# Kernel tuning notes

Measured on AMD Instinct MI355X. Metric: run time of the kernel, lower is better.

The kernel has to match this reference:

```python
import jax, jax.numpy as jnp
import numpy as np
from jax import lax

V, E, H = 32000, 256, 512
B, S, T = 32, 128, 64


def setup_inputs() -> dict:
    key = jax.random.key(0)
    ks = iter(jax.random.split(key, 32))
    p = lambda shape: jax.random.normal(next(ks), shape, jnp.float32) * 0.05
    inp = {
        "src": jax.random.randint(next(ks), (B, S), 0, V),
        "target": jax.random.randint(next(ks), (B, T), 0, V),
        "enc_emb": p((V, E)),
        "enc_Wih_f": p((3 * H, E)), "enc_Whh_f": p((3 * H, H)),
        "enc_bih_f": p((3 * H,)), "enc_bhh_f": p((3 * H,)),
        "enc_Wih_b": p((3 * H, E)), "enc_Whh_b": p((3 * H, H)),
        "enc_bih_b": p((3 * H,)), "enc_bhh_b": p((3 * H,)),
        "enc_fc_W": p((H, 2 * H)), "enc_fc_b": p((H,)),
        "dec_emb": p((V, E)),
        "attn_W": p((H, 3 * H)), "attn_b": p((H,)), "attn_v": p((H,)),
        "dec_Wih": p((3 * H, E + 2 * H)), "dec_Whh": p((3 * H, H)),
        "dec_bih": p((3 * H,)), "dec_bhh": p((3 * H,)),
        "fc1_W": p((V, 3 * H + E)), "fc1_b": p((V,)),
    }
    return inp


def gru_cell(h, x, Wih, Whh, bih, bhh):
    # PyTorch GRU cell. h:[B,H], x:[B,I]
    gx = x @ Wih.T + bih
    gh = h @ Whh.T + bhh
    xr, xz, xn = jnp.split(gx, 3, axis=-1)
    hr, hz, hn = jnp.split(gh, 3, axis=-1)
    r = jax.nn.sigmoid(xr + hr)
    z = jax.nn.sigmoid(xz + hz)
    n = jnp.tanh(xn + r * hn)
    return (1.0 - z) * n + z * h


def reference(src, target, enc_emb, enc_Wih_f, enc_Whh_f, enc_bih_f, enc_bhh_f,
              enc_Wih_b, enc_Whh_b, enc_bih_b, enc_bhh_b, enc_fc_W, enc_fc_b,
              dec_emb, attn_W, attn_b, attn_v, dec_Wih, dec_Whh, dec_bih,
              dec_bhh, fc1_W, fc1_b):
    src_t = src.T          # [S, B]
    tgt_t = target.T       # [T, B]
    batch = src.shape[0]
    hdim = enc_fc_b.shape[0]
    vocab = fc1_b.shape[0]
    tlen = target.shape[1]

    # ---- Encoder: bidirectional single-layer GRU ----
    x = enc_emb[src_t]     # [S, B, E]
    h0 = jnp.zeros((batch, hdim), x.dtype)

    def step_f(h, xt):
        h2 = gru_cell(h, xt, enc_Wih_f, enc_Whh_f, enc_bih_f, enc_bhh_f)
        return h2, h2

    def step_b(h, xt):
        h2 = gru_cell(h, xt, enc_Wih_b, enc_Whh_b, enc_bih_b, enc_bhh_b)
        return h2, h2

    hf, out_f = lax.scan(step_f, h0, x)
    hb, out_b_rev = lax.scan(step_b, h0, x[::-1])
    out_b = out_b_rev[::-1]
    enc_out = jnp.concatenate([out_f, out_b], axis=-1)        # [S, B, 2H]
    hidden = jnp.tanh(jnp.concatenate([hf, hb], axis=-1) @ enc_fc_W.T + enc_fc_b)  # [B, H]

    mask = (src != 0)                                          # [B, S]
    enc_bt = enc_out.transpose(1, 0, 2)                        # [B, S, 2H]
    # split additive-attention weight: cat order is (hidden, enc_out)
    W_h, W_e = attn_W[:, :hdim], attn_W[:, hdim:]
    enc_proj = jnp.einsum('bsd,hd->bsh', enc_bt, W_e)          # precompute [B,S,H]

    # ---- Decoder loop (teacher_ratio = 1.0 -> always teacher forcing) ----
    def dec_step(h, inp_tok):
        emb = dec_emb[inp_tok]                                 # [B, E]
        energy = jnp.tanh((h @ W_h.T)[:, None, :] + enc_proj + attn_b)  # [B,S,H]
        scores = energy @ attn_v                               # [B, S]
        scores = jnp.where(mask, scores, jnp.float32(-1e10))
        a = jax.nn.softmax(scores, axis=1)
        weighted = jnp.einsum('bs,bsd->bd', a, enc_bt)         # [B, 2H]
        gin = jnp.concatenate([emb, weighted], axis=-1)        # [B, E+2H]
        h2 = gru_cell(h, gin, dec_Wih, dec_Whh, dec_bih, dec_bhh)
        out = jnp.concatenate([h2, emb, weighted], axis=-1) @ fc1_W.T + fc1_b  # [B,V]
        return h2, (out, jnp.argmax(out, axis=1))

    _, (outs, preds) = lax.scan(dec_step, hidden, tgt_t[:-1])  # outs: [T-1, B, V]

    outputs = jnp.zeros((batch, tlen, vocab), outs.dtype).at[:, :tlen - 1, :].set(
        outs.transpose(1, 0, 2))
    preds_full = jnp.zeros((batch, tlen), jnp.float32).at[:, :tlen - 1].set(
        preds.T.astype(jnp.float32))
    return outputs, preds_full
```

## Files before the change

### kernel.cpp

```cpp
#include <hip/hip_runtime.h>

#define V_ 32000
#define E_ 256
#define H_ 512
#define B_ 32
#define S_ 128
#define T_ 64
#define TD_ 63
#define G3_ 1536
#define CATK_ 1792
#define DIN_ 1280
#define MPAD_ 2048

typedef __attribute__((ext_vector_type(8))) short bf16x8;
typedef __attribute__((ext_vector_type(4))) float f32x4;

__device__ inline unsigned short bf16_rne(float x) {
    unsigned u = __float_as_uint(x);
    unsigned r = u + 0x7FFFu + ((u >> 16) & 1u);
    return (unsigned short)(r >> 16);
}

__device__ __forceinline__ float ato_ldf(const float* p) {
    return __hip_atomic_load((const float*)p, __ATOMIC_RELAXED, __HIP_MEMORY_SCOPE_AGENT);
}
__device__ __forceinline__ void ato_stf(float* p, float v) {
    __hip_atomic_store(p, v, __ATOMIC_RELAXED, __HIP_MEMORY_SCOPE_AGENT);
}

__device__ __forceinline__ void fast_barN(unsigned* base, int idx, unsigned ngroups)
{
    asm volatile("s_waitcnt vmcnt(0)" ::: "memory");
    __syncthreads();
    if (threadIdx.x == 0) {
        unsigned* gcnt = base + (idx >> 4) * 64;
        unsigned* ggen = gcnt + 32;
        unsigned* tcnt = base + ngroups * 64;
        unsigned* tgen = tcnt + 32;
        unsigned g0 = __hip_atomic_load(ggen, __ATOMIC_RELAXED, __HIP_MEMORY_SCOPE_AGENT);
        unsigned a  = __hip_atomic_fetch_add(gcnt, 1u, __ATOMIC_RELAXED, __HIP_MEMORY_SCOPE_AGENT);
        if (a == 15u) {
            unsigned t0 = __hip_atomic_load(tgen, __ATOMIC_RELAXED, __HIP_MEMORY_SCOPE_AGENT);
            unsigned ta = __hip_atomic_fetch_add(tcnt, 1u, __ATOMIC_RELAXED, __HIP_MEMORY_SCOPE_AGENT);
            if (ta == ngroups - 1u) {
                __hip_atomic_store(tcnt, 0u, __ATOMIC_RELAXED, __HIP_MEMORY_SCOPE_AGENT);
                __hip_atomic_store(tgen, t0 + 1u, __ATOMIC_RELAXED, __HIP_MEMORY_SCOPE_AGENT);
            } else {
                while (__hip_atomic_load(tgen, __ATOMIC_RELAXED, __HIP_MEMORY_SCOPE_AGENT) == t0)
                    __builtin_amdgcn_s_sleep(1);
            }
            __hip_atomic_store(gcnt, 0u, __ATOMIC_RELAXED, __HIP_MEMORY_SCOPE_AGENT);
            __hip_atomic_store(ggen, g0 + 1u, __ATOMIC_RELAXED, __HIP_MEMORY_SCOPE_AGENT);
        } else {
            while (__hip_atomic_load(ggen, __ATOMIC_RELAXED, __HIP_MEMORY_SCOPE_AGENT) == g0)
                __builtin_amdgcn_s_sleep(1);
        }
    }
    __syncthreads();
}

__global__ __launch_bounds__(256)
void prep_kernel(const int* __restrict__ src, const int* __restrict__ tgt,
                 int* __restrict__ tokf, int* __restrict__ tokb, int* __restrict__ tokd,
                 float* __restrict__ enc_h0, unsigned* __restrict__ bars)
{
    int tid = blockIdx.x * 256 + threadIdx.x;
    if (tid < S_ * B_) {
        int s = tid >> 5, b = tid & 31;
        tokf[tid] = src[b * S_ + s];
        tokb[tid] = src[b * S_ + (S_ - 1 - s)];
    }
    if (tid < TD_ * B_) {
        int t = tid >> 5, b = tid & 31;
        tokd[tid] = tgt[b * T_ + t];
    }
    if (tid < 2 * B_ * H_) enc_h0[tid] = 0.f;
    if (tid < 4096) bars[tid] = 0u;
}

__global__ __launch_bounds__(256)
void emb_cat_kernel(const int* __restrict__ tokd, const float* __restrict__ dec_emb,
                    float* __restrict__ cat)
{
    int row = blockIdx.x;
    int tid = threadIdx.x;
    cat[(size_t)row * CATK_ + H_ + tid] = dec_emb[(size_t)tokd[row] * E_ + tid];
}

template<int GATHER, int FC1MAP>
__global__ __launch_bounds__(256)
void gemm128_kernel(const float* __restrict__ A, int lda,
                    const int* __restrict__ tokens, const float* __restrict__ emb,
                    const float* __restrict__ W, int ldw,
                    const float* __restrict__ bias,
                    float* __restrict__ C, int ldc,
                    int M, int N, int K)
{
    __shared__ float As[16][132];
    __shared__ float Ws[16][132];
    (void)N;
    int tid = threadIdx.x;
    int m0 = blockIdx.y * 128, n0 = blockIdx.x * 128;
    int tx = tid & 15, ty = tid >> 4;
    float c[8][8];
#pragma unroll
    for (int i = 0; i < 8; i++)
#pragma unroll
        for (int j = 0; j < 8; j++) c[i][j] = 0.f;

    int arow = tid >> 1;
    int kq = (tid & 1) * 8;

    int am = m0 + arow; if (am >= M) am = M - 1;
    const float* arp;
    if (GATHER) arp = emb + (size_t)tokens[am] * (size_t)K;
    else        arp = A + (size_t)am * (size_t)lda;
    const float* wrp = W + (size_t)(n0 + arow) * (size_t)ldw;

    for (int kb = 0; kb < K; kb += 16) {
        __syncthreads();
        float4 a0 = *(const float4*)(arp + kb + kq);
        float4 a1 = *(const float4*)(arp + kb + kq + 4);
        float4 w0 = *(const float4*)(wrp + kb + kq);
        float4 w1 = *(const float4*)(wrp + kb + kq + 4);
        As[kq + 0][arow] = a0.x; As[kq + 1][arow] = a0.y;
        As[kq + 2][arow] = a0.z; As[kq + 3][arow] = a0.w;
        As[kq + 4][arow] = a1.x; As[kq + 5][arow] = a1.y;
        As[kq + 6][arow] = a1.z; As[kq + 7][arow] = a1.w;
        Ws[kq + 0][arow] = w0.x; Ws[kq + 1][arow] = w0.y;
        Ws[kq + 2][arow] = w0.z; Ws[kq + 3][arow] = w0.w;
        Ws[kq + 4][arow] = w1.x; Ws[kq + 5][arow] = w1.y;
        Ws[kq + 6][arow] = w1.z; Ws[kq + 7][arow] = w1.w;
        __syncthreads();
#pragma unroll
        for (int kk = 0; kk < 16; kk++) {
            float a[8], bb[8];
            *(float4*)&a[0]  = *(const float4*)&As[kk][ty * 8];
            *(float4*)&a[4]  = *(const float4*)&As[kk][ty * 8 + 4];
            *(float4*)&bb[0] = *(const float4*)&Ws[kk][tx * 8];
            *(float4*)&bb[4] = *(const float4*)&Ws[kk][tx * 8 + 4];
#pragma unroll
            for (int i = 0; i < 8; i++)
#pragma unroll
                for (int j = 0; j < 8; j++) c[i][j] += a[i] * bb[j];
        }
    }

#pragma unroll
    for (int i = 0; i < 8; i++) {
        int m = m0 + ty * 8 + i;
        if (m < M) {
            size_t rowoff;
            if (FC1MAP) { int tt = m >> 5, bb2 = m & 31; rowoff = ((size_t)bb2 * T_ + tt) * (size_t)ldc; }
            else        rowoff = (size_t)m * (size_t)ldc;
#pragma unroll
            for (int j = 0; j < 8; j += 4) {
                int n = n0 + tx * 8 + j;
                float4 v;
                v.x = c[i][j + 0] + bias[n + 0];
                v.y = c[i][j + 1] + bias[n + 1];
                v.z = c[i][j + 2] + bias[n + 2];
                v.w = c[i][j + 3] + bias[n + 3];
                *(float4*)(C + rowoff + n) = v;
            }
        }
    }
}

__global__ __launch_bounds__(256)
void enc_coop_kernel(const float* __restrict__ gxf, const float* __restrict__ gxb,
                     const float* __restrict__ Whh_f, const float* __restrict__ bhh_f,
                     const float* __restrict__ Whh_b, const float* __restrict__ bhh_b,
                     float* __restrict__ encrot, float* __restrict__ enc_bt,
                     const float* __restrict__ fcW, const float* __restrict__ fcb,
                     float* __restrict__ hT0, unsigned* __restrict__ bars)
{
    const int bid = blockIdx.x;
    const int dir = bid >> 6, bh = (bid >> 5) & 1, kc = bid & 31;
    const int tid = threadIdx.x;
    const int bl = tid & 15, kl = tid >> 4;
    const int b = bh * 16 + bl, k = kc * 16 + kl;
    const float* Whh = dir ? Whh_b : Whh_f;
    const float* bhhp = dir ? bhh_b : bhh_f;
    const float* gx  = dir ? gxb : gxf;
    __shared__ float hL[16 * 516];
    const float* wr = Whh + (size_t)k * H_;
    const float* wz = Whh + (size_t)(H_ + k) * H_;
    const float* wn = Whh + (size_t)(2 * H_ + k) * H_;
    const float b_r = bhhp[k], b_z = bhhp[H_ + k], b_n = bhhp[2 * H_ + k];
    unsigned* dbar = bars + dir * 512;
    const int idx = bid & 63;

    for (int t = 0; t < S_; ++t) {
        const float* hin = encrot + (size_t)t * (2 * B_ * H_) + (size_t)dir * (B_ * H_);
        float* hout = encrot + (size_t)(t + 1) * (2 * B_ * H_) + (size_t)dir * (B_ * H_);
        const float* hsrc = hin + (size_t)bh * 16 * H_;
        for (int i = tid * 4; i < 16 * H_; i += 1024) {
            int r = i >> 9, cix = i & 511;
            *(float4*)&hL[r * 516 + cix] = *(const float4*)(hsrc + i);
        }
        __syncthreads();
        float ar = 0.f, az = 0.f, an = 0.f;
        const float* hv = &hL[bl * 516];
#pragma unroll 4
        for (int j = 0; j < H_; j += 4) {
            float4 h4 = *(const float4*)(hv + j);
            float4 r4 = *(const float4*)(wr + j);
            float4 z4 = *(const float4*)(wz + j);
            float4 n4 = *(const float4*)(wn + j);
            ar += h4.x * r4.x + h4.y * r4.y + h4.z * r4.z + h4.w * r4.w;
            az += h4.x * z4.x + h4.y * z4.y + h4.z * z4.z + h4.w * z4.w;
            an += h4.x * n4.x + h4.y * n4.y + h4.z * n4.z + h4.w * n4.w;
        }
        const float* gxr = gx + ((size_t)t * B_ + b) * G3_;
        float xr = gxr[k], xz = gxr[H_ + k], xn = gxr[2 * H_ + k];
        float rg = 1.f / (1.f + expf(-(xr + ar + b_r)));
        float zg = 1.f / (1.f + expf(-(xz + az + b_z)));
        float ng = tanhf(xn + rg * (an + b_n));
        float hp = hL[bl * 516 + k];
        float h2 = (1.f - zg) * ng + zg * hp;
        ato_stf(hout + (size_t)b * H_ + k, h2);
        int s_out = dir ? (S_ - 1 - t) : t;
        enc_bt[((size_t)b * S_ + s_out) * (2 * H_) + dir * H_ + k] = h2;
        fast_barN(dbar, idx, 4);
    }
    fast_barN(bars + 1024, bid, 8);

    {
        const int b2 = bid & 31, ih = bid >> 5;
        float* hc = hL;
        const float* hfin = encrot + (size_t)S_ * (2 * B_ * H_);
        const float* hf  = hfin + (size_t)b2 * H_;
        const float* hbk = hfin + (size_t)B_ * H_ + (size_t)b2 * H_;
        for (int i = tid; i < H_; i += 256) { hc[i] = hf[i]; hc[H_ + i] = hbk[i]; }
        __syncthreads();
        if (tid < 128) {
            int i = ih * 128 + tid;
            const float* w = fcW + (size_t)i * (2 * H_);
            float acc = 0.f;
            for (int j = 0; j < 2 * H_; j += 4) {
                float4 a4 = *(const float4*)&hc[j];
                float4 w4 = *(const float4*)(w + j);
                acc += a4.x * w4.x + a4.y * w4.y + a4.z * w4.z + a4.w * w4.w;
            }
            ato_stf(hT0 + (size_t)b2 * H_ + i, tanhf(acc + fcb[i]));
        }
    }
}

__global__ __launch_bounds__(256)
void dec_coop_kernel(const float* __restrict__ attn_W, const float* __restrict__ attn_v,
                     const float* __restrict__ enc_projB, const float* __restrict__ enc_bt,
                     const int* __restrict__ src,
                     const float* __restrict__ dWhh, const float* __restrict__ dbhh,
                     const float* __restrict__ dWih, const float* __restrict__ gx_emb,
                     float* __restrict__ cat, float* __restrict__ hT,
                     float* __restrict__ hwhT, float* __restrict__ wT,
                     float* __restrict__ wpart, float* __restrict__ mlq,
                     unsigned* __restrict__ bars)
{
    const int bid = blockIdx.x, tid = threadIdx.x;
    const int bp = bid >> 4, kr = bid & 15;
    const int b0 = bp * 2, b1 = b0 + 1;
    const int k0 = kr * 32;
    __shared__ float hA[512], hB[512];
    __shared__ float ghhA[96], ghhB[96];
    __shared__ float xwA[96], xwB[96];
    __shared__ float wA[1024], wB[1024];
    __shared__ float hwhL[512], vL[512], sL[32], eS[32], cmb[8];

    const int p1act = (kr < 8);
    const int p1q   = kr & 3;
    const int p1b_  = b0 + (kr >> 2);
    const int cact  = (kr == 8 || kr == 9);
    const int cb    = b0 + (kr - 8);
    const int r0 = tid >> 1, b2_0 = tid & 1;

    for (int t = 0; t < TD_; ++t) {
        const int pp = t & 1;
        const float* hin = hT + (size_t)pp * (B_ * H_);
        float* hout = hT + (size_t)(1 - pp) * (B_ * H_);
        float* cat_t = cat + (size_t)t * B_ * CATK_;

        for (int j = tid; j < H_; j += 256) {
            hA[j] = ato_ldf(hin + (size_t)b0 * H_ + j);
            hB[j] = ato_ldf(hin + (size_t)b1 * H_ + j);
        }
        __syncthreads();
        {
            const float* hv = b2_0 ? hB : hA;
            const float* wrow;
            if (r0 < 32) wrow = attn_W + (size_t)(k0 + r0) * G3_;
            else {
                int rr = r0 - 32;
                wrow = dWhh + (size_t)((rr >> 5) * H_ + k0 + (rr & 31)) * H_;
            }
            float a0 = 0.f, a1 = 0.f;
            for (int j = 0; j < H_; j += 8) {
                float4 w0 = *(const float4*)(wrow + j);
                float4 w1 = *(const float4*)(wrow + j + 4);
                float4 h0 = *(const float4*)&hv[j];
                float4 h1 = *(const float4*)&hv[j + 4];
                a0 += w0.x * h0.x + w0.y * h0.y + w0.z * h0.z + w0.w * h0.w;
                a1 += w1.x * h1.x + w1.y * h1.y + w1.z * h1.z + w1.w * h1.w;
            }
            float acc = a0 + a1;
            int b = b2_0 ? b1 : b0;
            if (r0 < 32) ato_stf(hwhT + (size_t)b * H_ + k0 + r0, acc);
            else {
                int rr = r0 - 32;
                float* g = b2_0 ? ghhB : ghhA;
                g[rr] = acc + dbhh[(rr >> 5) * H_ + k0 + (rr & 31)];
            }
        }
        fast_barN(bars, bid, 16);

        if (p1act) {
            const int ab = p1b_;
            const int s0 = p1q * 32;
            for (int i = tid; i < H_; i += 256) {
                hwhL[i] = ato_ldf(hwhT + (size_t)ab * H_ + i);
                vL[i] = attn_v[i];
            }
            __syncthreads();
            {
                int s = tid >> 3, u = tid & 7;
                const float* pr = enc_projB + ((size_t)ab * S_ + s0 + s) * H_ + u * 64;
                const float* hwo = hwhL + u * 64;
                const float* vo = vL + u * 64;
                float a0 = 0.f, a1 = 0.f, a2 = 0.f, a3 = 0.f;
#pragma unroll
                for (int i = 0; i < 64; i += 4) {
                    float x0 = hwo[i + 0] + pr[i + 0];
                    float x1 = hwo[i + 1] + pr[i + 1];
                    float x2 = hwo[i + 2] + pr[i + 2];
                    float x3 = hwo[i + 3] + pr[i + 3];
                    a0 += vo[i + 0] * (1.f - 2.f / (__expf(2.f * x0) + 1.f));
                    a1 += vo[i + 1] * (1.f - 2.f / (__expf(2.f * x1) + 1.f));
                    a2 += vo[i + 2] * (1.f - 2.f / (__expf(2.f * x2) + 1.f));
                    a3 += vo[i + 3] * (1.f - 2.f / (__expf(2.f * x3) + 1.f));
                }
                float acc = (a0 + a1) + (a2 + a3);
                acc += __shfl_xor(acc, 1);
                acc += __shfl_xor(acc, 2);
                acc += __shfl_xor(acc, 4);
                if (u == 0) sL[s] = (src[ab * S_ + s0 + s] != 0) ? acc : -1e10f;
            }
            __syncthreads();
            if (tid < 32) {
                float v = sL[tid];
                float m = v;
#pragma unroll
                for (int off = 1; off < 32; off <<= 1) m = fmaxf(m, __shfl_xor(m, off));
                float e = expf(v - m);
                eS[tid] = e;
                float l = e;
#pragma unroll
                for (int off = 1; off < 32; off <<= 1) l += __shfl_xor(l, off);
                if (tid == 0) {
                    ato_stf(mlq + (size_t)(ab * 4 + p1q) * 2 + 0, m);
                    ato_stf(mlq + (size_t)(ab * 4 + p1q) * 2 + 1, l);
                }
            }
            __syncthreads();
            {
                int c4 = tid * 4;
                const float* eb = enc_bt + ((size_t)ab * S_ + s0) * (2 * H_) + c4;
                float4 ac0 = {0, 0, 0, 0}, ac1 = {0, 0, 0, 0};
                float4 ac2 = {0, 0, 0, 0}, ac3 = {0, 0, 0, 0};
                for (int s = 0; s < 32; s += 4) {
                    float4 v0 = *(const float4*)(eb + (size_t)(s + 0) * (2 * H_));
                    float4 v1 = *(const float4*)(eb + (size_t)(s + 1) * (2 * H_));
                    float4 v2 = *(const float4*)(eb + (size_t)(s + 2) * (2 * H_));
                    float4 v3 = *(const float4*)(eb + (size_t)(s + 3) * (2 * H_));
                    float e0 = eS[s], e1 = eS[s + 1], e2 = eS[s + 2], e3 = eS[s + 3];
                    ac0.x += e0 * v0.x; ac0.y += e0 * v0.y; ac0.z += e0 * v0.z; ac0.w += e0 * v0.w;
                    ac1.x += e1 * v1.x; ac1.y += e1 * v1.y; ac1.z += e1 * v1.z; ac1.w += e1 * v1.w;
                    ac2.x += e2 * v2.x; ac2.y += e2 * v2.y; ac2.z += e2 * v2.z; ac2.w += e2 * v2.w;
                    ac3.x += e3 * v3.x; ac3.y += e3 * v3.y; ac3.z += e3 * v3.z; ac3.w += e3 * v3.w;
                }
                float* dst = wpart + (size_t)(ab * 4 + p1q) * 1024 + c4;
                ato_stf(dst + 0, (ac0.x + ac1.x) + (ac2.x + ac3.x));
                ato_stf(dst + 1, (ac0.y + ac1.y) + (ac2.y + ac3.y));
                ato_stf(dst + 2, (ac0.z + ac1.z) + (ac2.z + ac3.z));
                ato_stf(dst + 3, (ac0.w + ac1.w) + (ac2.w + ac3.w));
            }
        }
        fast_barN(bars, bid, 16);

        if (cact) {
            const int ab = cb;
            if (tid < 4) {
                cmb[tid] = ato_ldf(mlq + (size_t)(ab * 4 + tid) * 2 + 0);
                cmb[4 + tid] = ato_ldf(mlq + (size_t)(ab * 4 + tid) * 2 + 1);
            }
            __syncthreads();
            float m = fmaxf(fmaxf(cmb[0], cmb[1]), fmaxf(cmb[2], cmb[3]));
            float e0 = expf(cmb[0] - m), e1 = expf(cmb[1] - m);
            float e2 = expf(cmb[2] - m), e3 = expf(cmb[3] - m);
            float L = e0 * cmb[4] + e1 * cmb[5] + e2 * cmb[6] + e3 * cmb[7];
            float inv = 1.f / L;
            int c4 = tid * 4;
            const float* p0 = wpart + (size_t)(ab * 4 + 0) * 1024 + c4;
            const float* p1 = wpart + (size_t)(ab * 4 + 1) * 1024 + c4;
            const float* p2 = wpart + (size_t)(ab * 4 + 2) * 1024 + c4;
            const float* p3 = wpart + (size_t)(ab * 4 + 3) * 1024 + c4;
            float4 w4;
            w4.x = (e0 * ato_ldf(p0 + 0) + e1 * ato_ldf(p1 + 0) + e2 * ato_ldf(p2 + 0) + e3 * ato_ldf(p3 + 0)) * inv;
            w4.y = (e0 * ato_ldf(p0 + 1) + e1 * ato_ldf(p1 + 1) + e2 * ato_ldf(p2 + 1) + e3 * ato_ldf(p3 + 1)) * inv;
            w4.z = (e0 * ato_ldf(p0 + 2) + e1 * ato_ldf(p1 + 2) + e2 * ato_ldf(p2 + 2) + e3 * ato_ldf(p3 + 2)) * inv;
            w4.w = (e0 * ato_ldf(p0 + 3) + e1 * ato_ldf(p1 + 3) + e2 * ato_ldf(p2 + 3) + e3 * ato_ldf(p3 + 3)) * inv;
            ato_stf(wT + (size_t)ab * 1024 + c4 + 0, w4.x);
            ato_stf(wT + (size_t)ab * 1024 + c4 + 1, w4.y);
            ato_stf(wT + (size_t)ab * 1024 + c4 + 2, w4.z);
            ato_stf(wT + (size_t)ab * 1024 + c4 + 3, w4.w);
            *(float4*)(cat_t + (size_t)ab * CATK_ + (H_ + E_) + c4) = w4;
        }
        fast_barN(bars, bid, 16);

        for (int c = tid; c < 2 * H_; c += 256) {
            wA[c] = ato_ldf(wT + (size_t)b0 * 1024 + c);
            wB[c] = ato_ldf(wT + (size_t)b1 * 1024 + c);
        }
        __syncthreads();
        if (tid < 192) {
            int rr = tid >> 1, b2 = tid & 1;
            const float* wv = b2 ? wB : wA;
            const float* wrow = dWih + (size_t)((rr >> 5) * H_ + k0 + (rr & 31)) * DIN_ + E_;
            float a0 = 0.f, a1 = 0.f;
            for (int c = 0; c < 2 * H_; c += 8) {
                float4 w0 = *(const float4*)(wrow + c);
                float4 w1 = *(const float4*)(wrow + c + 4);
                float4 x0 = *(const float4*)&wv[c];
                float4 x1 = *(const float4*)&wv[c + 4];
                a0 += w0.x * x0.x + w0.y * x0.y + w0.z * x0.z + w0.w * x0.w;
                a1 += w1.x * x1.x + w1.y * x1.y + w1.z * x1.z + w1.w * x1.w;
            }
            (b2 ? xwB : xwA)[rr] = a0 + a1;
        }
        __syncthreads();
        if (tid < 64) {
            int b2 = tid >> 5, kk = tid & 31;
            int b = b2 ? b1 : b0;
            int k = k0 + kk;
            const float* g = b2 ? ghhB : ghhA;
            const float* x = b2 ? xwB : xwA;
            float hr = g[kk], hz = g[32 + kk], hn = g[64 + kk];
            float xr = x[kk], xz = x[32 + kk], xn = x[64 + kk];
            const float* gxe = gx_emb + ((size_t)t * B_ + b) * G3_;
            float rg = 1.f / (1.f + expf(-(gxe[k] + xr + hr)));
            float zg = 1.f / (1.f + expf(-(gxe[H_ + k] + xz + hz)));
            float ng = tanhf(gxe[2 * H_ + k] + xn + rg * hn);
            float hp = b2 ? hB[k] : hA[k];
            float h2 = (1.f - zg) * ng + zg * hp;
            ato_stf(hout + (size_t)b * H_ + k, h2);
            cat_t[(size_t)b * CATK_ + k] = h2;
        }
        fast_barN(bars, bid, 16);
    }
}

__global__ __launch_bounds__(256)
void splitA_kernel(const float* __restrict__ cat,
                   unsigned short* __restrict__ Ahi, unsigned short* __restrict__ Alo)
{
    size_t i4 = ((size_t)blockIdx.x * 256 + threadIdx.x) * 4;
    if (i4 >= (size_t)MPAD_ * CATK_) return;
    size_t row = i4 / CATK_;
    float4 v;
    if (row < (size_t)TD_ * B_) v = *(const float4*)(cat + i4);
    else { v.x = v.y = v.z = v.w = 0.f; }
    float f[4] = {v.x, v.y, v.z, v.w};
    unsigned short h[4], l[4];
#pragma unroll
    for (int j = 0; j < 4; j++) {
        h[j] = bf16_rne(f[j]);
        float hf = __uint_as_float((unsigned)h[j] << 16);
        l[j] = bf16_rne(f[j] - hf);
    }
    *(ushort4*)(Ahi + i4) = make_ushort4(h[0], h[1], h[2], h[3]);
    *(ushort4*)(Alo + i4) = make_ushort4(l[0], l[1], l[2], l[3]);
}

__global__ __launch_bounds__(256)
void fc1_mfma_kernel(const unsigned short* __restrict__ Ahi,
                     const unsigned short* __restrict__ Alo,
                     const float* __restrict__ W,
                     const float* __restrict__ bias,
                     float* __restrict__ C)
{
    __shared__ unsigned short lA[2][128][40];
    __shared__ unsigned short lW[2][128][40];
    const int tid = threadIdx.x;
    const int m0 = blockIdx.x * 128, n0 = blockIdx.y * 128;
    const int w = tid >> 6, lane = tid & 63;
    const int wm = w >> 1, wn = w & 1;
    const int frow = lane & 15, fk = (lane >> 4) * 8;

    f32x4 acc[4][4];
#pragma unroll
    for (int mi = 0; mi < 4; mi++)
#pragma unroll
        for (int ni = 0; ni < 4; ni++) acc[mi][ni] = (f32x4){0.f, 0.f, 0.f, 0.f};

    const int srow = tid >> 1;
    const int skq = (tid & 1) * 16;

    const unsigned short* gAhi = Ahi + (size_t)(m0 + srow) * CATK_ + skq;
    const unsigned short* gAlo = Alo + (size_t)(m0 + srow) * CATK_ + skq;
    const float*          gW   = W   + (size_t)(n0 + srow) * CATK_ + skq;

    int4 rAh0, rAh1, rAl0, rAl1;
    float4 rW0, rW1, rW2, rW3;

#define FC1_LOAD(kb)                                        \
    do {                                                    \
        rAh0 = *(const int4*)(gAhi + (kb));                 \
        rAh1 = *(const int4*)(gAhi + (kb) + 8);             \
        rAl0 = *(const int4*)(gAlo + (kb));                 \
        rAl1 = *(const int4*)(gAlo + (kb) + 8);             \
        rW0  = *(const float4*)(gW + (kb));                 \
        rW1  = *(const float4*)(gW + (kb) + 4);             \
        rW2  = *(const float4*)(gW + (kb) + 8);             \
        rW3  = *(const float4*)(gW + (kb) + 12);            \
    } while (0)

    FC1_LOAD(0);

    for (int kb = 0; kb < CATK_; kb += 32) {
        __syncthreads();
        *(int4*)&lA[0][srow][skq]     = rAh0;
        *(int4*)&lA[0][srow][skq + 8] = rAh1;
        *(int4*)&lA[1][srow][skq]     = rAl0;
        *(int4*)&lA[1][srow][skq + 8] = rAl1;
        {
            float f[16] = {rW0.x, rW0.y, rW0.z, rW0.w, rW1.x, rW1.y, rW1.z, rW1.w,
                           rW2.x, rW2.y, rW2.z, rW2.w, rW3.x, rW3.y, rW3.z, rW3.w};
            unsigned hp[8], lp[8];
#pragma unroll
            for (int j = 0; j < 8; j++) {
                float x0 = f[2 * j], x1 = f[2 * j + 1];
                unsigned short h0 = bf16_rne(x0), h1 = bf16_rne(x1);
                float r0 = x0 - __uint_as_float((unsigned)h0 << 16);
                float r1 = x1 - __uint_as_float((unsigned)h1 << 16);
                hp[j] = (unsigned)h0 | ((unsigned)h1 << 16);
                lp[j] = (unsigned)bf16_rne(r0) | ((unsigned)bf16_rne(r1) << 16);
            }
            *(int4*)&lW[0][srow][skq]     = make_int4(hp[0], hp[1], hp[2], hp[3]);
            *(int4*)&lW[0][srow][skq + 8] = make_int4(hp[4], hp[5], hp[6], hp[7]);
            *(int4*)&lW[1][srow][skq]     = make_int4(lp[0], lp[1], lp[2], lp[3]);
            *(int4*)&lW[1][srow][skq + 8] = make_int4(lp[4], lp[5], lp[6], lp[7]);
        }
        __syncthreads();
        if (kb + 32 < CATK_) FC1_LOAD(kb + 32);

        bf16x8 a[2][4];
#pragma unroll
        for (int mi = 0; mi < 4; mi++) {
            int r = wm * 64 + mi * 16 + frow;
            a[0][mi] = *(const bf16x8*)&lA[0][r][fk];
            a[1][mi] = *(const bf16x8*)&lA[1][r][fk];
        }
#pragma unroll
        for (int ni = 0; ni < 4; ni++) {
            int r = wn * 64 + ni * 16 + frow;
            bf16x8 bh = *(const bf16x8*)&lW[0][r][fk];
            bf16x8 bl = *(const bf16x8*)&lW[1][r][fk];
#pragma unroll
            for (int mi = 0; mi < 4; mi++) {
                acc[mi][ni] = __builtin_amdgcn_mfma_f32_16x16x32_bf16(a[0][mi], bh, acc[mi][ni], 0, 0, 0);
                acc[mi][ni] = __builtin_amdgcn_mfma_f32_16x16x32_bf16(a[1][mi], bh, acc[mi][ni], 0, 0, 0);
                acc[mi][ni] = __builtin_amdgcn_mfma_f32_16x16x32_bf16(a[0][mi], bl, acc[mi][ni], 0, 0, 0);
            }
        }
    }
#undef FC1_LOAD

#pragma unroll
    for (int ni = 0; ni < 4; ni++) {
        int col = n0 + wn * 64 + ni * 16 + frow;
        float bc = bias[col];
#pragma unroll
        for (int mi = 0; mi < 4; mi++) {
            int mbase = m0 + wm * 64 + mi * 16 + (lane >> 4) * 4;
            f32x4 v = acc[mi][ni];
#pragma unroll
            for (int r = 0; r < 4; r++) {
                int m = mbase + r;
                if (m < TD_ * B_) {
                    int tt = m >> 5, bb2 = m & 31;
                    C[((size_t)bb2 * T_ + tt) * V_ + col] = v[r] + bc;
                }
            }
        }
    }
}

__global__ __launch_bounds__(256)
void argmax_kernel(const float* __restrict__ outp, float* __restrict__ preds)
{
    int row = blockIdx.x;
    int t = row >> 5, b = row & 31;
    const float* p = outp + ((size_t)b * T_ + t) * V_;
    int tid = threadIdx.x;
    float best = -3.4e38f; int bi = V_;
    for (int i = tid; i < V_; i += 256) {
        float v = p[i];
        if (v > best) { best = v; bi = i; }
    }
    __shared__ float bv[256];
    __shared__ int bidx[256];
    bv[tid] = best; bidx[tid] = bi;
    __syncthreads();
    for (int off = 128; off > 0; off >>= 1) {
        if (tid < off) {
            float v2 = bv[tid + off]; int i2 = bidx[tid + off];
            if (v2 > bv[tid] || (v2 == bv[tid] && i2 < bidx[tid])) { bv[tid] = v2; bidx[tid] = i2; }
        }
        __syncthreads();
    }
    if (tid == 0) preds[(size_t)b * T_ + t] = (float)bidx[0];
}

__global__ __launch_bounds__(256)
void zero_tail_kernel(float* __restrict__ outp, float* __restrict__ preds)
{
    int tid = blockIdx.x * 256 + threadIdx.x;
    if (tid < B_ * V_) {
        int b = tid / V_;
        int c = tid % V_;
        outp[((size_t)b * T_ + (T_ - 1)) * V_ + c] = 0.f;
    }
    if (tid < B_) preds[(size_t)tid * T_ + (T_ - 1)] = 0.f;
}

extern "C" void kernel_launch(void* const* d_in, const int* in_sizes, int n_in,
                              void* d_out, int out_size, void* d_ws, size_t ws_size,
                              hipStream_t stream)
{
    (void)in_sizes; (void)n_in; (void)out_size;
    const int*   src     = (const int*)d_in[0];
    const int*   tgt     = (const int*)d_in[1];
    const float* enc_emb = (const float*)d_in[2];
    const float* Wih_f   = (const float*)d_in[3];
    const float* Whh_f   = (const float*)d_in[4];
    const float* bih_f   = (const float*)d_in[5];
    const float* bhh_f   = (const float*)d_in[6];
    const float* Wih_b   = (const float*)d_in[7];
    const float* Whh_b   = (const float*)d_in[8];
    const float* bih_b   = (const float*)d_in[9];
    const float* bhh_b   = (const float*)d_in[10];
    const float* fcW     = (const float*)d_in[11];
    const float* fcb     = (const float*)d_in[12];
    const float* dec_emb = (const float*)d_in[13];
    const float* attn_W  = (const float*)d_in[14];
    const float* attn_b  = (const float*)d_in[15];
    const float* attn_v  = (const float*)d_in[16];
    const float* dWih    = (const float*)d_in[17];
    const float* dWhh    = (const float*)d_in[18];
    const float* dbih    = (const float*)d_in[19];
    const float* dbhh    = (const float*)d_in[20];
    const float* fc1W    = (const float*)d_in[21];
    const float* fc1b    = (const float*)d_in[22];
    (void)dbih;

    float* ws     = (float*)d_ws;
    float* cat    = ws;
    float* gx_emb = cat + (size_t)TD_ * B_ * CATK_;
    int*   tokf   = (int*)(gx_emb + (size_t)TD_ * B_ * G3_);
    int*   tokb   = tokf + 4096;
    int*   tokd   = tokb + 4096;
    unsigned* bars = (unsigned*)(tokd + 4096);
    unsigned short* Ahi = (unsigned short*)(bars + 4096);
    unsigned short* Alo = Ahi + (size_t)MPAD_ * CATK_;
    size_t ws_req = (size_t)((char*)(Alo + (size_t)MPAD_ * CATK_) - (char*)d_ws);
    const bool use_mfma = (ws_size >= ws_req);

    float* dout      = (float*)d_out;
    float* gxf       = dout;
    float* gxb       = gxf + (size_t)S_ * B_ * G3_;
    float* enc_bt    = gxb + (size_t)S_ * B_ * G3_;
    float* enc_projB = enc_bt + (size_t)B_ * S_ * 2 * H_;
    float* encrot    = enc_projB + (size_t)B_ * S_ * H_;
    float* hT        = encrot + (size_t)(S_ + 1) * 2 * B_ * H_;
    float* hwhT      = hT + 2 * B_ * H_;
    float* wT        = hwhT + B_ * H_;
    float* wpart     = wT + 2 * B_ * H_;
    float* mlq       = wpart + (size_t)B_ * 4 * 1024;
    float* preds     = dout + (size_t)B_ * T_ * V_;

    dim3 thr(256);

    hipLaunchKernelGGL(prep_kernel, dim3(256), thr, 0, stream,
                       src, tgt, tokf, tokb, tokd, encrot, bars);
    hipLaunchKernelGGL(emb_cat_kernel, dim3(TD_ * B_), thr, 0, stream, tokd, dec_emb, cat);

    hipLaunchKernelGGL((gemm128_kernel<1, 0>), dim3(G3_ / 128, (S_ * B_) / 128), thr, 0, stream,
                       (const float*)nullptr, 0, tokf, enc_emb, Wih_f, E_, bih_f,
                       gxf, G3_, S_ * B_, G3_, E_);
    hipLaunchKernelGGL((gemm128_kernel<1, 0>), dim3(G3_ / 128, (S_ * B_) / 128), thr, 0, stream,
                       (const float*)nullptr, 0, tokb, enc_emb, Wih_b, E_, bih_b,
                       gxb, G3_, S_ * B_, G3_, E_);

    hipLaunchKernelGGL(enc_coop_kernel, dim3(128), thr, 0, stream,
                       gxf, gxb, Whh_f, bhh_f, Whh_b, bhh_b, encrot, enc_bt,
                       fcW, fcb, hT , bars);

    hipLaunchKernelGGL((gemm128_kernel<0, 0>), dim3(H_ / 128, (B_ * S_) / 128), thr, 0, stream,
                       enc_bt, 2 * H_, (const int*)nullptr, (const float*)nullptr,
                       attn_W + H_, G3_, attn_b, enc_projB, H_, B_ * S_, H_, 2 * H_);

    hipLaunchKernelGGL((gemm128_kernel<1, 0>), dim3(G3_ / 128, (TD_ * B_ + 127) / 128), thr, 0, stream,
                       (const float*)nullptr, 0, tokd, dec_emb, dWih, DIN_, dbih,
                       gx_emb, G3_, TD_ * B_, G3_, E_);

    hipLaunchKernelGGL(dec_coop_kernel, dim3(256), thr, 0, stream,
                       attn_W, attn_v, enc_projB, enc_bt, src,
                       dWhh, dbhh, dWih, gx_emb, cat, hT, hwhT, wT, wpart, mlq,
                       bars + 2048);

    if (use_mfma) {
        hipLaunchKernelGGL(splitA_kernel, dim3((MPAD_ * CATK_ / 4 + 255) / 256), thr, 0, stream,
                           cat, Ahi, Alo);
        hipLaunchKernelGGL(fc1_mfma_kernel, dim3(MPAD_ / 128, V_ / 128), thr, 0, stream,
                           Ahi, Alo, fc1W, fc1b, dout);
    } else {
        hipLaunchKernelGGL((gemm128_kernel<0, 1>), dim3(V_ / 128, (TD_ * B_ + 127) / 128), thr, 0, stream,
                           cat, CATK_, (const int*)nullptr, (const float*)nullptr,
                           fc1W, CATK_, fc1b, dout, V_, TD_ * B_, V_, CATK_);
    }

    hipLaunchKernelGGL(argmax_kernel, dim3(TD_ * B_), thr, 0, stream, dout, preds);
    hipLaunchKernelGGL(zero_tail_kernel, dim3((B_ * V_ + 255) / 256), thr, 0, stream, dout, preds);
}
```

Before: 6.063 ms.

## Split decoder attention over all 16 blocks per batch pair with 8 sequence chunks

```diff
diff --git a/kernel.cpp b/kernel.cpp
--- a/kernel.cpp
+++ b/kernel.cpp
@@ -267,13 +267,13 @@
     __shared__ float ghhA[96], ghhB[96];
     __shared__ float xwA[96], xwB[96];
     __shared__ float wA[1024], wB[1024];
-    __shared__ float hwhL[512], vL[512], sL[32], eS[32], cmb[8];
-
-    const int p1act = (kr < 8);
-    const int p1q   = kr & 3;
-    const int p1b_  = b0 + (kr >> 2);
-    const int cact  = (kr == 8 || kr == 9);
-    const int cb    = b0 + (kr - 8);
+    __shared__ float hwP[8 * 68], vP[8 * 68];
+    __shared__ float sL[16], eS[16], cmb[16];
+
+    const int p1ab = b0 + (kr & 1);
+    const int p1q  = kr >> 1;
+    const int cact = (kr == 8 || kr == 9);
+    const int cb   = b0 + (kr - 8);
     const int r0 = tid >> 1, b2_0 = tid & 1;
 
     for (int t = 0; t < TD_; ++t) {
@@ -315,30 +315,32 @@
         }
         fast_barN(bars, bid, 16);
 
-        if (p1act) {
-            const int ab = p1b_;
-            const int s0 = p1q * 32;
+        {
+            const int ab = p1ab;
+            const int s0 = p1q * 16;
             for (int i = tid; i < H_; i += 256) {
-                hwhL[i] = ato_ldf(hwhT + (size_t)ab * H_ + i);
-                vL[i] = attn_v[i];
+                int pi = (i >> 6) * 68 + (i & 63);
+                hwP[pi] = ato_ldf(hwhT + (size_t)ab * H_ + i);
+                vP[pi]  = attn_v[i];
             }
             __syncthreads();
-            {
+            if (tid < 128) {
                 int s = tid >> 3, u = tid & 7;
                 const float* pr = enc_projB + ((size_t)ab * S_ + s0 + s) * H_ + u * 64;
-                const float* hwo = hwhL + u * 64;
-                const float* vo = vL + u * 64;
+                const float* hwo = hwP + u * 68;
+                const float* vo  = vP + u * 68;
                 float a0 = 0.f, a1 = 0.f, a2 = 0.f, a3 = 0.f;
 #pragma unroll
                 for (int i = 0; i < 64; i += 4) {
-                    float x0 = hwo[i + 0] + pr[i + 0];
-                    float x1 = hwo[i + 1] + pr[i + 1];
-                    float x2 = hwo[i + 2] + pr[i + 2];
-                    float x3 = hwo[i + 3] + pr[i + 3];
-                    a0 += vo[i + 0] * (1.f - 2.f / (__expf(2.f * x0) + 1.f));
-                    a1 += vo[i + 1] * (1.f - 2.f / (__expf(2.f * x1) + 1.f));
-                    a2 += vo[i + 2] * (1.f - 2.f / (__expf(2.f * x2) + 1.f));
-                    a3 += vo[i + 3] * (1.f - 2.f / (__expf(2.f * x3) + 1.f));
+                    float4 p4 = *(const float4*)(pr + i);
+                    float4 h4 = *(const float4*)(hwo + i);
+                    float4 v4 = *(const float4*)(vo + i);
+                    float x0 = h4.x + p4.x, x1 = h4.y + p4.y;
+                    float x2 = h4.z + p4.z, x3 = h4.w + p4.w;
+                    a0 += v4.x * (1.f - 2.f / (__expf(2.f * x0) + 1.f));
+                    a1 += v4.y * (1.f - 2.f / (__expf(2.f * x1) + 1.f));
+                    a2 += v4.z * (1.f - 2.f / (__expf(2.f * x2) + 1.f));
+                    a3 += v4.w * (1.f - 2.f / (__expf(2.f * x3) + 1.f));
                 }
                 float acc = (a0 + a1) + (a2 + a3);
                 acc += __shfl_xor(acc, 1);
@@ -347,19 +349,19 @@
                 if (u == 0) sL[s] = (src[ab * S_ + s0 + s] != 0) ? acc : -1e10f;
             }
             __syncthreads();
-            if (tid < 32) {
+            if (tid < 16) {
                 float v = sL[tid];
                 float m = v;
 #pragma unroll
-                for (int off = 1; off < 32; off <<= 1) m = fmaxf(m, __shfl_xor(m, off));
+                for (int off = 1; off < 16; off <<= 1) m = fmaxf(m, __shfl_xor(m, off));
                 float e = expf(v - m);
                 eS[tid] = e;
                 float l = e;
 #pragma unroll
-                for (int off = 1; off < 32; off <<= 1) l += __shfl_xor(l, off);
+                for (int off = 1; off < 16; off <<= 1) l += __shfl_xor(l, off);
                 if (tid == 0) {
-                    ato_stf(mlq + (size_t)(ab * 4 + p1q) * 2 + 0, m);
-                    ato_stf(mlq + (size_t)(ab * 4 + p1q) * 2 + 1, l);
+                    ato_stf(mlq + (size_t)(ab * 8 + p1q) * 2 + 0, m);
+                    ato_stf(mlq + (size_t)(ab * 8 + p1q) * 2 + 1, l);
                 }
             }
             __syncthreads();
@@ -368,7 +370,8 @@
                 const float* eb = enc_bt + ((size_t)ab * S_ + s0) * (2 * H_) + c4;
                 float4 ac0 = {0, 0, 0, 0}, ac1 = {0, 0, 0, 0};
                 float4 ac2 = {0, 0, 0, 0}, ac3 = {0, 0, 0, 0};
-                for (int s = 0; s < 32; s += 4) {
+#pragma unroll
+                for (int s = 0; s < 16; s += 4) {
                     float4 v0 = *(const float4*)(eb + (size_t)(s + 0) * (2 * H_));
                     float4 v1 = *(const float4*)(eb + (size_t)(s + 1) * (2 * H_));
                     float4 v2 = *(const float4*)(eb + (size_t)(s + 2) * (2 * H_));
@@ -379,7 +382,7 @@
                     ac2.x += e2 * v2.x; ac2.y += e2 * v2.y; ac2.z += e2 * v2.z; ac2.w += e2 * v2.w;
                     ac3.x += e3 * v3.x; ac3.y += e3 * v3.y; ac3.z += e3 * v3.z; ac3.w += e3 * v3.w;
                 }
-                float* dst = wpart + (size_t)(ab * 4 + p1q) * 1024 + c4;
+                float* dst = wpart + (size_t)(p1ab * 8 + p1q) * 1024 + c4;
                 ato_stf(dst + 0, (ac0.x + ac1.x) + (ac2.x + ac3.x));
                 ato_stf(dst + 1, (ac0.y + ac1.y) + (ac2.y + ac3.y));
                 ato_stf(dst + 2, (ac0.z + ac1.z) + (ac2.z + ac3.z));
@@ -390,26 +393,29 @@
 
         if (cact) {
             const int ab = cb;
-            if (tid < 4) {
-                cmb[tid] = ato_ldf(mlq + (size_t)(ab * 4 + tid) * 2 + 0);
-                cmb[4 + tid] = ato_ldf(mlq + (size_t)(ab * 4 + tid) * 2 + 1);
+            if (tid < 8) {
+                cmb[tid] = ato_ldf(mlq + (size_t)(ab * 8 + tid) * 2 + 0);
+                cmb[8 + tid] = ato_ldf(mlq + (size_t)(ab * 8 + tid) * 2 + 1);
             }
             __syncthreads();
-            float m = fmaxf(fmaxf(cmb[0], cmb[1]), fmaxf(cmb[2], cmb[3]));
-            float e0 = expf(cmb[0] - m), e1 = expf(cmb[1] - m);
-            float e2 = expf(cmb[2] - m), e3 = expf(cmb[3] - m);
-            float L = e0 * cmb[4] + e1 * cmb[5] + e2 * cmb[6] + e3 * cmb[7];
+            float m = cmb[0];
+#pragma unroll
+            for (int j = 1; j < 8; j++) m = fmaxf(m, cmb[j]);
+            float e[8]; float L = 0.f;
+#pragma unroll
+            for (int j = 0; j < 8; j++) { e[j] = expf(cmb[j] - m); L += e[j] * cmb[8 + j]; }
             float inv = 1.f / L;
             int c4 = tid * 4;
-            const float* p0 = wpart + (size_t)(ab * 4 + 0) * 1024 + c4;
-            const float* p1 = wpart + (size_t)(ab * 4 + 1) * 1024 + c4;
-            const float* p2 = wpart + (size_t)(ab * 4 + 2) * 1024 + c4;
-            const float* p3 = wpart + (size_t)(ab * 4 + 3) * 1024 + c4;
-            float4 w4;
-            w4.x = (e0 * ato_ldf(p0 + 0) + e1 * ato_ldf(p1 + 0) + e2 * ato_ldf(p2 + 0) + e3 * ato_ldf(p3 + 0)) * inv;
-            w4.y = (e0 * ato_ldf(p0 + 1) + e1 * ato_ldf(p1 + 1) + e2 * ato_ldf(p2 + 1) + e3 * ato_ldf(p3 + 1)) * inv;
-            w4.z = (e0 * ato_ldf(p0 + 2) + e1 * ato_ldf(p1 + 2) + e2 * ato_ldf(p2 + 2) + e3 * ato_ldf(p3 + 2)) * inv;
-            w4.w = (e0 * ato_ldf(p0 + 3) + e1 * ato_ldf(p1 + 3) + e2 * ato_ldf(p2 + 3) + e3 * ato_ldf(p3 + 3)) * inv;
+            float4 w4 = {0, 0, 0, 0};
+#pragma unroll
+            for (int j = 0; j < 8; j++) {
+                const float* p = wpart + (size_t)(ab * 8 + j) * 1024 + c4;
+                w4.x += e[j] * ato_ldf(p + 0);
+                w4.y += e[j] * ato_ldf(p + 1);
+                w4.z += e[j] * ato_ldf(p + 2);
+                w4.w += e[j] * ato_ldf(p + 3);
+            }
+            w4.x *= inv; w4.y *= inv; w4.z *= inv; w4.w *= inv;
             ato_stf(wT + (size_t)ab * 1024 + c4 + 0, w4.x);
             ato_stf(wT + (size_t)ab * 1024 + c4 + 1, w4.y);
             ato_stf(wT + (size_t)ab * 1024 + c4 + 2, w4.z);
@@ -686,7 +692,7 @@
     float* hwhT      = hT + 2 * B_ * H_;
     float* wT        = hwhT + B_ * H_;
     float* wpart     = wT + 2 * B_ * H_;
-    float* mlq       = wpart + (size_t)B_ * 4 * 1024;
+    float* mlq       = wpart + (size_t)B_ * 8 * 1024;
     float* preds     = dout + (size_t)B_ * T_ * V_;
 
     dim3 thr(256);
```

Measured after the change: 6.334 ms. 1.04x slower.

## Repartition encoder GRU by batch pairs to use small per-group barriers

Applied to the files above, without the earlier changes.

```diff
diff --git a/kernel.cpp b/kernel.cpp
--- a/kernel.cpp
+++ b/kernel.cpp
@@ -28,31 +28,20 @@
     __hip_atomic_store(p, v, __ATOMIC_RELAXED, __HIP_MEMORY_SCOPE_AGENT);
 }
 
-__device__ __forceinline__ void fast_barN(unsigned* base, int idx, unsigned ngroups)
+__device__ __forceinline__ void group_bar(unsigned* gbase, unsigned nb)
 {
     asm volatile("s_waitcnt vmcnt(0)" ::: "memory");
     __syncthreads();
     if (threadIdx.x == 0) {
-        unsigned* gcnt = base + (idx >> 4) * 64;
-        unsigned* ggen = gcnt + 32;
-        unsigned* tcnt = base + ngroups * 64;
-        unsigned* tgen = tcnt + 32;
-        unsigned g0 = __hip_atomic_load(ggen, __ATOMIC_RELAXED, __HIP_MEMORY_SCOPE_AGENT);
-        unsigned a  = __hip_atomic_fetch_add(gcnt, 1u, __ATOMIC_RELAXED, __HIP_MEMORY_SCOPE_AGENT);
-        if (a == 15u) {
-            unsigned t0 = __hip_atomic_load(tgen, __ATOMIC_RELAXED, __HIP_MEMORY_SCOPE_AGENT);
-            unsigned ta = __hip_atomic_fetch_add(tcnt, 1u, __ATOMIC_RELAXED, __HIP_MEMORY_SCOPE_AGENT);
-            if (ta == ngroups - 1u) {
-                __hip_atomic_store(tcnt, 0u, __ATOMIC_RELAXED, __HIP_MEMORY_SCOPE_AGENT);
-                __hip_atomic_store(tgen, t0 + 1u, __ATOMIC_RELAXED, __HIP_MEMORY_SCOPE_AGENT);
-            } else {
-                while (__hip_atomic_load(tgen, __ATOMIC_RELAXED, __HIP_MEMORY_SCOPE_AGENT) == t0)
-                    __builtin_amdgcn_s_sleep(1);
-            }
-            __hip_atomic_store(gcnt, 0u, __ATOMIC_RELAXED, __HIP_MEMORY_SCOPE_AGENT);
-            __hip_atomic_store(ggen, g0 + 1u, __ATOMIC_RELAXED, __HIP_MEMORY_SCOPE_AGENT);
+        unsigned* cnt = gbase;
+        unsigned* gen = gbase + 32;
+        unsigned g0 = __hip_atomic_load(gen, __ATOMIC_RELAXED, __HIP_MEMORY_SCOPE_AGENT);
+        unsigned a  = __hip_atomic_fetch_add(cnt, 1u, __ATOMIC_RELAXED, __HIP_MEMORY_SCOPE_AGENT);
+        if (a == nb - 1u) {
+            __hip_atomic_store(cnt, 0u, __ATOMIC_RELAXED, __HIP_MEMORY_SCOPE_AGENT);
+            __hip_atomic_store(gen, g0 + 1u, __ATOMIC_RELAXED, __HIP_MEMORY_SCOPE_AGENT);
         } else {
-            while (__hip_atomic_load(ggen, __ATOMIC_RELAXED, __HIP_MEMORY_SCOPE_AGENT) == g0)
+            while (__hip_atomic_load(gen, __ATOMIC_RELAXED, __HIP_MEMORY_SCOPE_AGENT) == g0)
                 __builtin_amdgcn_s_sleep(1);
         }
     }
@@ -62,7 +51,7 @@
 __global__ __launch_bounds__(256)
 void prep_kernel(const int* __restrict__ src, const int* __restrict__ tgt,
                  int* __restrict__ tokf, int* __restrict__ tokb, int* __restrict__ tokd,
-                 float* __restrict__ enc_h0, unsigned* __restrict__ bars)
+                 float* __restrict__ h_enc, unsigned* __restrict__ bars)
 {
     int tid = blockIdx.x * 256 + threadIdx.x;
     if (tid < S_ * B_) {
@@ -74,7 +63,7 @@
         int t = tid >> 5, b = tid & 31;
         tokd[tid] = tgt[b * T_ + t];
     }
-    if (tid < 2 * B_ * H_) enc_h0[tid] = 0.f;
+    if (tid < 2 * 2 * B_ * H_) h_enc[tid] = 0.f;
     if (tid < 4096) bars[tid] = 0u;
 }
 
@@ -171,71 +160,93 @@
 void enc_coop_kernel(const float* __restrict__ gxf, const float* __restrict__ gxb,
                      const float* __restrict__ Whh_f, const float* __restrict__ bhh_f,
                      const float* __restrict__ Whh_b, const float* __restrict__ bhh_b,
-                     float* __restrict__ encrot, float* __restrict__ enc_bt,
+                     float* __restrict__ h_enc, float* __restrict__ enc_bt,
                      const float* __restrict__ fcW, const float* __restrict__ fcb,
                      float* __restrict__ hT0, unsigned* __restrict__ bars)
 {
-    const int bid = blockIdx.x;
-    const int dir = bid >> 6, bh = (bid >> 5) & 1, kc = bid & 31;
-    const int tid = threadIdx.x;
-    const int bl = tid & 15, kl = tid >> 4;
-    const int b = bh * 16 + bl, k = kc * 16 + kl;
-    const float* Whh = dir ? Whh_b : Whh_f;
-    const float* bhhp = dir ? bhh_b : bhh_f;
-    const float* gx  = dir ? gxb : gxf;
-    __shared__ float hL[16 * 516];
-    const float* wr = Whh + (size_t)k * H_;
-    const float* wz = Whh + (size_t)(H_ + k) * H_;
-    const float* wn = Whh + (size_t)(2 * H_ + k) * H_;
-    const float b_r = bhhp[k], b_z = bhhp[H_ + k], b_n = bhhp[2 * H_ + k];
-    unsigned* dbar = bars + dir * 512;
-    const int idx = bid & 63;
+    const int bid = blockIdx.x, tid = threadIdx.x;
+    const int bp = bid >> 3, kq = bid & 7;
+    const int b0 = bp * 2, b1 = b0 + 1;
+    const int k0 = kq * 64;
+    __shared__ float hS[4][512];
+    __shared__ float egA[384], egB[384];
+    unsigned* gbar = bars + bp * 64;
 
     for (int t = 0; t < S_; ++t) {
-        const float* hin = encrot + (size_t)t * (2 * B_ * H_) + (size_t)dir * (B_ * H_);
-        float* hout = encrot + (size_t)(t + 1) * (2 * B_ * H_) + (size_t)dir * (B_ * H_);
-        const float* hsrc = hin + (size_t)bh * 16 * H_;
-        for (int i = tid * 4; i < 16 * H_; i += 1024) {
-            int r = i >> 9, cix = i & 511;
-            *(float4*)&hL[r * 516 + cix] = *(const float4*)(hsrc + i);
-        }
-        __syncthreads();
-        float ar = 0.f, az = 0.f, an = 0.f;
-        const float* hv = &hL[bl * 516];
-#pragma unroll 4
-        for (int j = 0; j < H_; j += 4) {
-            float4 h4 = *(const float4*)(hv + j);
-            float4 r4 = *(const float4*)(wr + j);
-            float4 z4 = *(const float4*)(wz + j);
-            float4 n4 = *(const float4*)(wn + j);
-            ar += h4.x * r4.x + h4.y * r4.y + h4.z * r4.z + h4.w * r4.w;
-            az += h4.x * z4.x + h4.y * z4.y + h4.z * z4.z + h4.w * z4.w;
-            an += h4.x * n4.x + h4.y * n4.y + h4.z * n4.z + h4.w * n4.w;
-        }
-        const float* gxr = gx + ((size_t)t * B_ + b) * G3_;
-        float xr = gxr[k], xz = gxr[H_ + k], xn = gxr[2 * H_ + k];
-        float rg = 1.f / (1.f + expf(-(xr + ar + b_r)));
-        float zg = 1.f / (1.f + expf(-(xz + az + b_z)));
-        float ng = tanhf(xn + rg * (an + b_n));
-        float hp = hL[bl * 516 + k];
-        float h2 = (1.f - zg) * ng + zg * hp;
-        ato_stf(hout + (size_t)b * H_ + k, h2);
-        int s_out = dir ? (S_ - 1 - t) : t;
-        enc_bt[((size_t)b * S_ + s_out) * (2 * H_) + dir * H_ + k] = h2;
-        fast_barN(dbar, idx, 4);
-    }
-    fast_barN(bars + 1024, bid, 8);
+        const int pp = t & 1;
+        const float* hin0 = h_enc + (size_t)(0 * 2 + pp) * B_ * H_;
+        const float* hin1 = h_enc + (size_t)(1 * 2 + pp) * B_ * H_;
+        for (int j = tid; j < H_; j += 256) {
+            hS[0][j] = ato_ldf(hin0 + (size_t)b0 * H_ + j);
+            hS[1][j] = ato_ldf(hin0 + (size_t)b1 * H_ + j);
+            hS[2][j] = ato_ldf(hin1 + (size_t)b0 * H_ + j);
+            hS[3][j] = ato_ldf(hin1 + (size_t)b1 * H_ + j);
+        }
+        __syncthreads();
+        for (int r = tid; r < 384; r += 256) {
+            int dir = r / 192, rr = r - dir * 192;
+            int grow = (rr >> 6) * H_ + k0 + (rr & 63);
+            const float* wrow = (dir ? Whh_b : Whh_f) + (size_t)grow * H_;
+            const float* h0 = hS[dir * 2 + 0];
+            const float* h1 = hS[dir * 2 + 1];
+            float a00 = 0.f, a01 = 0.f, a10 = 0.f, a11 = 0.f;
+            for (int j = 0; j < H_; j += 8) {
+                float4 w0 = *(const float4*)(wrow + j);
+                float4 w1 = *(const float4*)(wrow + j + 4);
+                float4 x0 = *(const float4*)&h0[j];
+                float4 x1 = *(const float4*)&h0[j + 4];
+                float4 y0 = *(const float4*)&h1[j];
+                float4 y1 = *(const float4*)&h1[j + 4];
+                a00 += w0.x * x0.x + w0.y * x0.y + w0.z * x0.z + w0.w * x0.w;
+                a01 += w1.x * x1.x + w1.y * x1.y + w1.z * x1.z + w1.w * x1.w;
+                a10 += w0.x * y0.x + w0.y * y0.y + w0.z * y0.z + w0.w * y0.w;
+                a11 += w1.x * y1.x + w1.y * y1.y + w1.z * y1.z + w1.w * y1.w;
+            }
+            float bb = (dir ? bhh_b : bhh_f)[grow];
+            egA[r] = a00 + a01 + bb;
+            egB[r] = a10 + a11 + bb;
+        }
+        __syncthreads();
+        {
+            int dir = tid >> 7, b2 = (tid >> 6) & 1, kk = tid & 63;
+            int k = k0 + kk;
+            int b = b2 ? b1 : b0;
+            int rb = dir * 192;
+            const float* eg = b2 ? egB : egA;
+            float hr = eg[rb + kk], hz = eg[rb + 64 + kk], hn = eg[rb + 128 + kk];
+            const float* gx = dir ? gxb : gxf;
+            const float* gxr = gx + ((size_t)t * B_ + b) * G3_;
+            float xr = gxr[k], xz = gxr[H_ + k], xn = gxr[2 * H_ + k];
+            float rg = 1.f / (1.f + expf(-(xr + hr)));
+            float zg = 1.f / (1.f + expf(-(xz + hz)));
+            float ng = tanhf(xn + rg * hn);
+            float hp = hS[dir * 2 + b2][k];
+            float h2 = (1.f - zg) * ng + zg * hp;
+            float* hout = h_enc + (size_t)(dir * 2 + 1 - pp) * B_ * H_;
+            ato_stf(hout + (size_t)b * H_ + k, h2);
+            int s_out = dir ? (S_ - 1 - t) : t;
+            enc_bt[((size_t)b * S_ + s_out) * (2 * H_) + dir * H_ + k] = h2;
+        }
+        group_bar(gbar, 8);
+    }
 
     {
-        const int b2 = bid & 31, ih = bid >> 5;
-        float* hc = hL;
-        const float* hfin = encrot + (size_t)S_ * (2 * B_ * H_);
-        const float* hf  = hfin + (size_t)b2 * H_;
-        const float* hbk = hfin + (size_t)B_ * H_ + (size_t)b2 * H_;
-        for (int i = tid; i < H_; i += 256) { hc[i] = hf[i]; hc[H_ + i] = hbk[i]; }
+        float* hc0 = &hS[0][0];
+        float* hc1 = &hS[2][0];
+        const float* hf0 = h_enc + (size_t)0 * B_ * H_;
+        const float* hf1 = h_enc + (size_t)2 * B_ * H_;
+        for (int j = tid; j < H_; j += 256) {
+            hc0[j] = ato_ldf(hf0 + (size_t)b0 * H_ + j);
+            hc0[H_ + j] = ato_ldf(hf1 + (size_t)b0 * H_ + j);
+            hc1[j] = ato_ldf(hf0 + (size_t)b1 * H_ + j);
+            hc1[H_ + j] = ato_ldf(hf1 + (size_t)b1 * H_ + j);
+        }
         __syncthreads();
         if (tid < 128) {
-            int i = ih * 128 + tid;
+            int b2 = tid >> 6, ii = tid & 63;
+            int i = k0 + ii;
+            int b = b2 ? b1 : b0;
+            const float* hc = b2 ? hc1 : hc0;
             const float* w = fcW + (size_t)i * (2 * H_);
             float acc = 0.f;
             for (int j = 0; j < 2 * H_; j += 4) {
@@ -243,7 +254,7 @@
                 float4 w4 = *(const float4*)(w + j);
                 acc += a4.x * w4.x + a4.y * w4.y + a4.z * w4.z + a4.w * w4.w;
             }
-            ato_stf(hT0 + (size_t)b2 * H_ + i, tanhf(acc + fcb[i]));
+            ato_stf(hT0 + (size_t)b * H_ + i, tanhf(acc + fcb[i]));
         }
     }
 }
@@ -267,11 +278,13 @@
     __shared__ float ghhA[96], ghhB[96];
     __shared__ float xwA[96], xwB[96];
     __shared__ float wA[1024], wB[1024];
-    __shared__ float hwhL[512], vL[512], sL[32], eS[32], cmb[8];
+    __shared__ float hwP[8 * 68], vP[8 * 68];
+    __shared__ float sL[32], eS[32], cmb[8];
+    unsigned* gbar = bars + bp * 64;
 
     const int p1act = (kr < 8);
+    const int p1ab  = b0 + (kr >> 2);
     const int p1q   = kr & 3;
-    const int p1b_  = b0 + (kr >> 2);
     const int cact  = (kr == 8 || kr == 9);
     const int cb    = b0 + (kr - 8);
     const int r0 = tid >> 1, b2_0 = tid & 1;
@@ -313,32 +326,34 @@
                 g[rr] = acc + dbhh[(rr >> 5) * H_ + k0 + (rr & 31)];
             }
         }
-        fast_barN(bars, bid, 16);
+        group_bar(gbar, 16);
 
         if (p1act) {
-            const int ab = p1b_;
+            const int ab = p1ab;
             const int s0 = p1q * 32;
             for (int i = tid; i < H_; i += 256) {
-                hwhL[i] = ato_ldf(hwhT + (size_t)ab * H_ + i);
-                vL[i] = attn_v[i];
+                int pi = (i >> 6) * 68 + (i & 63);
+                hwP[pi] = ato_ldf(hwhT + (size_t)ab * H_ + i);
+                vP[pi]  = attn_v[i];
             }
             __syncthreads();
             {
                 int s = tid >> 3, u = tid & 7;
                 const float* pr = enc_projB + ((size_t)ab * S_ + s0 + s) * H_ + u * 64;
-                const float* hwo = hwhL + u * 64;
-                const float* vo = vL + u * 64;
+                const float* hwo = hwP + u * 68;
+                const float* vo  = vP + u * 68;
                 float a0 = 0.f, a1 = 0.f, a2 = 0.f, a3 = 0.f;
 #pragma unroll
                 for (int i = 0; i < 64; i += 4) {
-                    float x0 = hwo[i + 0] + pr[i + 0];
-                    float x1 = hwo[i + 1] + pr[i + 1];
-                    float x2 = hwo[i + 2] + pr[i + 2];
-                    float x3 = hwo[i + 3] + pr[i + 3];
-                    a0 += vo[i + 0] * (1.f - 2.f / (__expf(2.f * x0) + 1.f));
-                    a1 += vo[i + 1] * (1.f - 2.f / (__expf(2.f * x1) + 1.f));
-                    a2 += vo[i + 2] * (1.f - 2.f / (__expf(2.f * x2) + 1.f));
-                    a3 += vo[i + 3] * (1.f - 2.f / (__expf(2.f * x3) + 1.f));
+                    float4 p4 = *(const float4*)(pr + i);
+                    float4 h4 = *(const float4*)(hwo + i);
+                    float4 v4 = *(const float4*)(vo + i);
+                    float x0 = h4.x + p4.x, x1 = h4.y + p4.y;
+                    float x2 = h4.z + p4.z, x3 = h4.w + p4.w;
+                    a0 += v4.x * (1.f - 2.f / (__expf(2.f * x0) + 1.f));
+                    a1 += v4.y * (1.f - 2.f / (__expf(2.f * x1) + 1.f));
+                    a2 += v4.z * (1.f - 2.f / (__expf(2.f * x2) + 1.f));
+                    a3 += v4.w * (1.f - 2.f / (__expf(2.f * x3) + 1.f));
                 }
                 float acc = (a0 + a1) + (a2 + a3);
                 acc += __shfl_xor(acc, 1);
@@ -386,7 +401,7 @@
                 ato_stf(dst + 3, (ac0.w + ac1.w) + (ac2.w + ac3.w));
             }
         }
-        fast_barN(bars, bid, 16);
+        group_bar(gbar, 16);
 
         if (cact) {
             const int ab = cb;
@@ -416,7 +431,7 @@
             ato_stf(wT + (size_t)ab * 1024 + c4 + 3, w4.w);
             *(float4*)(cat_t + (size_t)ab * CATK_ + (H_ + E_) + c4) = w4;
         }
-        fast_barN(bars, bid, 16);
+        group_bar(gbar, 16);
 
         for (int c = tid; c < 2 * H_; c += 256) {
             wA[c] = ato_ldf(wT + (size_t)b0 * 1024 + c);
@@ -456,7 +471,7 @@
             ato_stf(hout + (size_t)b * H_ + k, h2);
             cat_t[(size_t)b * CATK_ + k] = h2;
         }
-        fast_barN(bars, bid, 16);
+        group_bar(gbar, 16);
     }
 }
 
@@ -681,8 +696,8 @@
     float* gxb       = gxf + (size_t)S_ * B_ * G3_;
     float* enc_bt    = gxb + (size_t)S_ * B_ * G3_;
     float* enc_projB = enc_bt + (size_t)B_ * S_ * 2 * H_;
-    float* encrot    = enc_projB + (size_t)B_ * S_ * H_;
-    float* hT        = encrot + (size_t)(S_ + 1) * 2 * B_ * H_;
+    float* h_enc     = enc_projB + (size_t)B_ * S_ * H_;
+    float* hT        = h_enc + 4 * B_ * H_;
     float* hwhT      = hT + 2 * B_ * H_;
     float* wT        = hwhT + B_ * H_;
     float* wpart     = wT + 2 * B_ * H_;
@@ -692,7 +707,7 @@
     dim3 thr(256);
 
     hipLaunchKernelGGL(prep_kernel, dim3(256), thr, 0, stream,
-                       src, tgt, tokf, tokb, tokd, encrot, bars);
+                       src, tgt, tokf, tokb, tokd, h_enc, bars);
     hipLaunchKernelGGL(emb_cat_kernel, dim3(TD_ * B_), thr, 0, stream, tokd, dec_emb, cat);
 
     hipLaunchKernelGGL((gemm128_kernel<1, 0>), dim3(G3_ / 128, (S_ * B_) / 128), thr, 0, stream,
@@ -703,7 +718,7 @@
                        gxb, G3_, S_ * B_, G3_, E_);
 
     hipLaunchKernelGGL(enc_coop_kernel, dim3(128), thr, 0, stream,
-                       gxf, gxb, Whh_f, bhh_f, Whh_b, bhh_b, encrot, enc_bt,
+                       gxf, gxb, Whh_f, bhh_f, Whh_b, bhh_b, h_enc, enc_bt,
                        fcW, fcb, hT , bars);
 
     hipLaunchKernelGGL((gemm128_kernel<0, 0>), dim3(H_ / 128, (B_ * S_) / 128), thr, 0, stream,
```

Result: slower. 7.435 ms (+22.6%).
